# Performance work log

Hardware: AMD Instinct MI355X
Metric: run time of the kernel (lower is better)

## Reference

```python
import jax, jax.numpy as jnp
import numpy as np

KS = 3
N = KS * KS  # 9 kernel taps
EPS = 1e-5
LEAK = 0.1


def _conv2d(x, w, b=None, stride=1, pad=1):
    out = jax.lax.conv_general_dilated(
        x, w, (stride, stride), [(pad, pad), (pad, pad)],
        dimension_numbers=('NCHW', 'OIHW', 'NCHW'))
    if b is not None:
        out = out + b[None, :, None, None]
    return out


def setup_inputs() -> dict:
    key = jax.random.key(0)
    k1, k2, k3, k4 = jax.random.split(key, 4)
    b, c_in, c_out, H, W = 4, 128, 256, 128, 128
    x = jax.random.normal(k1, (b, c_in, H, W), dtype=jnp.float32)
    # offset-predicting conv (torch inits it to zero; small random keeps
    # sampling near-grid but nontrivial)
    p_w = jax.random.normal(k2, (2 * N, c_in, KS, KS), dtype=jnp.float32) * 0.01
    p_b = jnp.zeros((2 * N,), dtype=jnp.float32)
    # main conv weight (bias=False in DeformConv2d)
    w_conv = jax.random.normal(k3, (c_out, c_in, KS, KS), dtype=jnp.float32) * 0.05
    gamma = jnp.ones((c_out,), dtype=jnp.float32)
    beta = jnp.zeros((c_out,), dtype=jnp.float32)
    return {"x": x, "p_w": p_w, "p_b": p_b, "w_conv": w_conv,
            "gamma": gamma, "beta": beta}


def reference(x, p_w, p_b, w_conv, gamma, beta):
    b, c, H, W = x.shape
    # offsets: (b, 2N, H, W); first N channels = x-offsets, last N = y-offsets
    off = jnp.transpose(_conv2d(x, p_w, p_b), (0, 2, 3, 1))  # (b,h,w,2N)
    off_x, off_y = off[..., :N], off[..., N:]

    x_pad = jnp.pad(x, ((0, 0), (0, 0), (1, 1), (1, 1)))  # zero_padding(1)
    Hp, Wp = H + 2, W + 2

    # p = p_0 + p_n + offset (in padded coordinates)
    dx = jnp.repeat(jnp.arange(-1, 2), KS).astype(x.dtype)  # (9,)
    dy = jnp.tile(jnp.arange(-1, 2), KS).astype(x.dtype)
    p0x = jnp.arange(1, H + 1, dtype=x.dtype)[None, :, None, None]
    p0y = jnp.arange(1, W + 1, dtype=x.dtype)[None, None, :, None]
    px = p0x + dx + off_x  # (b,h,w,N)
    py = p0y + dy + off_y

    fx, fy = jnp.floor(px), jnp.floor(py)
    qlt_x = jnp.clip(fx, 0, Hp - 1)
    qlt_y = jnp.clip(fy, 0, Wp - 1)
    qrb_x = jnp.clip(fx + 1, 0, Hp - 1)
    qrb_y = jnp.clip(fy + 1, 0, Wp - 1)

    pcx = jnp.clip(px, 0, Hp - 1)
    pcy = jnp.clip(py, 0, Wp - 1)

    # bilinear weights (matches original g_lt/g_rb/g_lb/g_rt)
    g_lt = (1 + (qlt_x - pcx)) * (1 + (qlt_y - pcy))
    g_rb = (1 - (qrb_x - pcx)) * (1 - (qrb_y - pcy))
    g_lb = (1 + (qlt_x - pcx)) * (1 - (qrb_y - pcy))
    g_rt = (1 - (qrb_x - pcx)) * (1 + (qlt_y - pcy))

    x_flat = x_pad.reshape(b, c, Hp * Wp)
    ilt_x, ilt_y = qlt_x.astype(jnp.int32), qlt_y.astype(jnp.int32)
    irb_x, irb_y = qrb_x.astype(jnp.int32), qrb_y.astype(jnp.int32)

    def samp(ix, iy, g):
        idx = (ix * Wp + iy).reshape(b, -1)  # (b, h*w*N)
        v = jnp.take_along_axis(x_flat, idx[:, None, :], axis=2)
        return g[:, None] * v.reshape(b, c, H, W, N)

    x_off = (samp(ilt_x, ilt_y, g_lt) + samp(irb_x, irb_y, g_rb)
             + samp(ilt_x, irb_y, g_lb) + samp(irb_x, ilt_y, g_rt))

    # equivalent to reshaping to (b,c,3h,3w) and conv(k=3,s=3), bias=False
    out = jnp.einsum('bchwn,ocn->bohw', x_off,
                     w_conv.reshape(w_conv.shape[0], c, N))

    # BatchNorm2d (training-mode batch stats, biased var) + LeakyReLU(0.1)
    mean = out.mean(axis=(0, 2, 3), keepdims=True)
    var = ((out - mean) ** 2).mean(axis=(0, 2, 3), keepdims=True)
    out = (out - mean) * jax.lax.rsqrt(var + EPS)
    out = out * gamma[None, :, None, None] + beta[None, :, None, None]
    return jnp.where(out >= 0, out, LEAK * out)
```

## Files before the change

kernel.cpp:

```cpp
#include <hip/hip_runtime.h>
#include <cstdint>

typedef __attribute__((ext_vector_type(8))) short bf16x8;
typedef __attribute__((ext_vector_type(4))) float f32x4;

#define B_   4
#define C_   128
#define H_   128
#define W_   128
#define HP_  130
#define WP_  130
#define O_   256
#define HW_  (H_*W_)

#define XPAD_BYTES   (B_*HP_*WP_*C_*2)
#define OFF_BYTE     XPAD_BYTES
#define OFF_BYTES    (B_*HW_*18*4)
#define WREPB_BYTE   (OFF_BYTE + OFF_BYTES)
#define WREPB_BYTES  (9*C_*O_*2)
#define STATS_BYTE   (WREPB_BYTE + WREPB_BYTES)
#define WOFF_BYTE    (STATS_BYTE + 4096)
#define WOFF_BYTES   (9*4*4*32*8*2)

typedef __attribute__((address_space(1))) const void gconst_void;
typedef __attribute__((address_space(3))) void lds_void;
#define GLD_LDS16(gp, lp) __builtin_amdgcn_global_load_lds((gconst_void*)(gp), (lds_void*)(lp), 16, 0, 0)

__device__ __forceinline__ unsigned pack_bf2(float a, float b) {
    unsigned ua = __builtin_bit_cast(unsigned, a) + 0x8000u;
    unsigned ub = __builtin_bit_cast(unsigned, b) + 0x8000u;
    return __builtin_amdgcn_perm(ub, ua, 0x07060302u);
}

__global__ void k_transpose(const float* __restrict__ x, unsigned short* __restrict__ xpad) {
    __shared__ float tile[32][33];
    int w0 = blockIdx.x * 32, c0 = blockIdx.y * 32;
    int bh = blockIdx.z;
    int b = bh >> 7, h = bh & 127;
    int tx = threadIdx.x, ty = threadIdx.y;
#pragma unroll
    for (int i = 0; i < 4; i++) {
        int c = c0 + ty + i * 8;
        tile[ty + i * 8][tx] = x[((b * C_ + c) * H_ + h) * W_ + w0 + tx];
    }
    __syncthreads();
    int tid = ty * 32 + tx;
    int cp = tid & 15;
    int wl = tid >> 4;
#pragma unroll
    for (int i = 0; i < 2; i++) {
        int wll = wl + i * 16;
        int w = w0 + wll;
        unsigned v = pack_bf2(tile[2 * cp][wll], tile[2 * cp + 1][wll]);
        *(unsigned*)(&xpad[((size_t)((b * HP_ + h + 1) * WP_ + (w + 1))) * C_ + c0 + 2 * cp]) = v;
    }
}

__global__ void k_repack2(const float* __restrict__ p_w, short* __restrict__ wofff) {
    int i = blockIdx.x * 256 + threadIdx.x;
    if (i < 9 * 4096) {
        int e = i & 7, m = (i >> 3) & 31, q = (i >> 8) & 3, kc = (i >> 10) & 3, tap = i >> 12;
        float f = (m < 18) ? p_w[((size_t)m * C_ + kc * 32 + q * 8 + e) * 9 + tap] : 0.f;
        unsigned u = __builtin_bit_cast(unsigned, f);
        u += 0x7fffu + ((u >> 16) & 1u);
        wofff[i] = (short)(u >> 16);
    }
}

__global__ __launch_bounds__(256) void k_offconv(const unsigned short* __restrict__ xpad,
                                                 const short* __restrict__ wofff,
                                                 const float* __restrict__ p_b,
                                                 float* __restrict__ offT) {
    int t = threadIdx.x;
    int ph = blockIdx.x;
    int h  = blockIdx.y;
    int b  = blockIdx.z;
    const unsigned short* xb = xpad + (size_t)b * HP_ * WP_ * C_;
    int lane = t & 63, wv = t >> 6;
    int q = lane >> 4, l15 = lane & 15;
    int pos0 = ph * 64 + wv * 16;
    int poscol = pos0 + l15;

    f32x4 accA = {0.f, 0.f, 0.f, 0.f}, accB = {0.f, 0.f, 0.f, 0.f};
    const bf16x8* Wf = (const bf16x8*)wofff;

    for (int tap = 0; tap < 9; tap++) {
        int row = h + tap / 3;
        int col = poscol + tap % 3;
        const unsigned short* src = xb + ((size_t)(row * WP_ + col)) * C_ + q * 8;
#pragma unroll
        for (int kc = 0; kc < 4; kc++) {
            bf16x8 a0 = Wf[(size_t)(((tap * 4 + kc) * 4 + q) * 32) + l15];
            bf16x8 a1 = Wf[(size_t)(((tap * 4 + kc) * 4 + q) * 32) + 16 + l15];
            bf16x8 bv = *(const bf16x8*)(src + kc * 32);
            accA = __builtin_amdgcn_mfma_f32_16x16x32_bf16(a0, bv, accA, 0, 0, 0);
            accB = __builtin_amdgcn_mfma_f32_16x16x32_bf16(a1, bv, accB, 0, 0, 0);
        }
    }
    size_t hw = (size_t)h * W_ + pos0 + l15;
#pragma unroll
    for (int r = 0; r < 4; r++) {
        int j = q * 4 + r;
        offT[((size_t)(b * 18 + j)) * HW_ + hw] = accA[r] + p_b[j];
    }
    if (q == 0) {
#pragma unroll
        for (int r = 0; r < 2; r++) {
            int j = 16 + r;
            offT[((size_t)(b * 18 + j)) * HW_ + hw] = accB[r] + p_b[j];
        }
    }
}

__global__ void k_repack(const float* __restrict__ w_conv, unsigned short* __restrict__ wrepb) {
    int i = blockIdx.x * 256 + threadIdx.x;
    if (i < 9 * C_ * O_) {
        int ki8 = i & 7;
        int o   = (i >> 3) & 255;
        int kq  = (i >> 11) & 3;
        int kc  = (i >> 13) & 3;
        int n   = i >> 15;
        int c = kc * 32 + kq * 8 + ki8;
        float f = w_conv[(o * C_ + c) * 9 + n];
        unsigned u = __builtin_bit_cast(unsigned, f);
        u += 0x7fffu + ((u >> 16) & 1u);
        wrepb[i] = (unsigned short)(u >> 16);
    }
}

__global__ __launch_bounds__(512, 4) void k_main(const unsigned short* __restrict__ xpad,
                                                 const float* __restrict__ offT,
                                                 const unsigned short* __restrict__ wrepb,
                                                 float* __restrict__ out,
                                                 float* __restrict__ stats) {
    __shared__ short Wl[2][8192];
    __shared__ short Vl[2][4128];
    __shared__ int   pbase[2][4][128];
    __shared__ float pg[2][4][128];
    __shared__ float red0[256], red1[256];

    int t = threadIdx.x;
    int i_blk = blockIdx.x;
    int b = i_blk & 3;
    int h = i_blk >> 2;
    const unsigned short* xb = xpad + (size_t)b * HP_ * WP_ * C_;

    int lane = t & 63, wv = t >> 6;
    int q = lane >> 4, l15 = lane & 15;
    int m0 = (wv & 3) * 64;
    int ph = wv >> 2;
    int n0 = ph * 64;
    int c4g = t & 3, posb = t >> 2;

    auto OFFSETS = [&](int n, int pb) {
        if (t < 128) {
            int w = t;
            float offx = offT[((size_t)(b * 18 + n)) * HW_ + h * W_ + w];
            float offy = offT[((size_t)(b * 18 + 9 + n)) * HW_ + h * W_ + w];
            int dxn = n / 3 - 1, dyn = n % 3 - 1;
            float px = (float)(h + 1 + dxn) + offx;
            float py = (float)(w + 1 + dyn) + offy;
            float pcx = fminf(fmaxf(px, 0.f), 129.f);
            float pcy = fminf(fmaxf(py, 0.f), 129.f);
            float fx = floorf(px), fy = floorf(py);
            float q0x = fminf(fmaxf(fx, 0.f), 129.f);
            float q0y = fminf(fmaxf(fy, 0.f), 129.f);
            float q1x = fminf(fmaxf(fx + 1.f, 0.f), 129.f);
            float q1y = fminf(fmaxf(fy + 1.f, 0.f), 129.f);
            float wx0 = 1.f + (q0x - pcx), wx1 = 1.f - (q1x - pcx);
            float wy0 = 1.f + (q0y - pcy), wy1 = 1.f - (q1y - pcy);
            int i0x = (int)q0x, i0y = (int)q0y, i1x = (int)q1x, i1y = (int)q1y;
            pbase[pb][0][w] = (i0x * WP_ + i0y) * C_;
            pbase[pb][1][w] = (i1x * WP_ + i1y) * C_;
            pbase[pb][2][w] = (i0x * WP_ + i1y) * C_;
            pbase[pb][3][w] = (i1x * WP_ + i0y) * C_;
            pg[pb][0][w] = wx0 * wy0;
            pg[pb][1][w] = wx1 * wy1;
            pg[pb][2][w] = wx0 * wy1;
            pg[pb][3][w] = wx1 * wy0;
        }
    };

    f32x4 acc[4][4];
#pragma unroll
    for (int i = 0; i < 4; i++)
#pragma unroll
        for (int j = 0; j < 4; j++) acc[i][j] = (f32x4){0.f, 0.f, 0.f, 0.f};

    OFFSETS(0, 0);
    __syncthreads();

    {
        const unsigned short* ws = wrepb;
        GLD_LDS16(ws + (size_t)t * 8, &Wl[0][wv * 512]);
        GLD_LDS16(ws + (size_t)(t + 512) * 8, &Wl[0][wv * 512 + 4096]);
        int cof = c4g * 8;
        uint4 A  = *(const uint4*)(xb + pbase[0][0][posb] + cof);
        uint4 Bv = *(const uint4*)(xb + pbase[0][1][posb] + cof);
        uint4 Cv = *(const uint4*)(xb + pbase[0][2][posb] + cof);
        uint4 Dv = *(const uint4*)(xb + pbase[0][3][posb] + cof);
        float g0 = pg[0][0][posb], g1 = pg[0][1][posb], g2 = pg[0][2][posb], g3 = pg[0][3][posb];
        unsigned outw[4];
#pragma unroll
        for (int k = 0; k < 4; k++) {
            unsigned ua = (&A.x)[k], ub = (&Bv.x)[k], uc = (&Cv.x)[k], ud = (&Dv.x)[k];
            float alo = __builtin_bit_cast(float, ua << 16), ahi = __builtin_bit_cast(float, ua & 0xffff0000u);
            float blo = __builtin_bit_cast(float, ub << 16), bhi = __builtin_bit_cast(float, ub & 0xffff0000u);
            float clo = __builtin_bit_cast(float, uc << 16), chi = __builtin_bit_cast(float, uc & 0xffff0000u);
            float dlo = __builtin_bit_cast(float, ud << 16), dhi = __builtin_bit_cast(float, ud & 0xffff0000u);
            float vlo = g0 * alo + g1 * blo + g2 * clo + g3 * dlo;
            float vhi = g0 * ahi + g1 * bhi + g2 * chi + g3 * dhi;
            outw[k] = pack_bf2(vlo, vhi);
        }
        *(uint4*)&Vl[0][(unsigned)(c4g * 129 + posb) * 8] = make_uint4(outw[0], outw[1], outw[2], outw[3]);
    }
    __syncthreads();

#pragma unroll 1
    for (int s = 0; s < 36; s++) {
        int cur = s & 1, nxt = cur ^ 1;
        uint4 A, Bv, Cv, Dv;
        float g0 = 0.f, g1 = 0.f, g2 = 0.f, g3 = 0.f;
        bool st = (s < 35);
        if (st) {
            int s1 = s + 1;
            const unsigned short* ws = wrepb + (size_t)s1 * 8192;
            GLD_LDS16(ws + (size_t)t * 8, &Wl[nxt][wv * 512]);
            GLD_LDS16(ws + (size_t)(t + 512) * 8, &Wl[nxt][wv * 512 + 4096]);
            int n1 = s1 >> 2, kc1 = s1 & 3, pb1 = n1 & 1;
            int cof = kc1 * 32 + c4g * 8;
            A  = *(const uint4*)(xb + pbase[pb1][0][posb] + cof);
            Bv = *(const uint4*)(xb + pbase[pb1][1][posb] + cof);
            Cv = *(const uint4*)(xb + pbase[pb1][2][posb] + cof);
            Dv = *(const uint4*)(xb + pbase[pb1][3][posb] + cof);
            g0 = pg[pb1][0][posb]; g1 = pg[pb1][1][posb];
            g2 = pg[pb1][2][posb]; g3 = pg[pb1][3][posb];
        }
        {
            const bf16x8* Af = (const bf16x8*)Wl[cur];
            const bf16x8* Bf = (const bf16x8*)Vl[cur];
            bf16x8 av[4];
#pragma unroll
            for (int i = 0; i < 4; i++) av[i] = Af[q * 256 + m0 + i * 16 + l15];
            __builtin_amdgcn_s_setprio(1);
#pragma unroll
            for (int j = 0; j < 4; j++) {
                bf16x8 bv = Bf[q * 129 + n0 + j * 16 + l15];
#pragma unroll
                for (int i = 0; i < 4; i++)
                    acc[i][j] = __builtin_amdgcn_mfma_f32_16x16x32_bf16(av[i], bv, acc[i][j], 0, 0, 0);
            }
            __builtin_amdgcn_s_setprio(0);
        }
        if ((s & 3) == 2) {
            int n = s >> 2;
            if (n < 8) OFFSETS(n + 1, (n + 1) & 1);
        }
        if (st) {
            unsigned outw[4];
#pragma unroll
            for (int k = 0; k < 4; k++) {
                unsigned ua = (&A.x)[k], ub = (&Bv.x)[k], uc = (&Cv.x)[k], ud = (&Dv.x)[k];
                float alo = __builtin_bit_cast(float, ua << 16), ahi = __builtin_bit_cast(float, ua & 0xffff0000u);
                float blo = __builtin_bit_cast(float, ub << 16), bhi = __builtin_bit_cast(float, ub & 0xffff0000u);
                float clo = __builtin_bit_cast(float, uc << 16), chi = __builtin_bit_cast(float, uc & 0xffff0000u);
                float dlo = __builtin_bit_cast(float, ud << 16), dhi = __builtin_bit_cast(float, ud & 0xffff0000u);
                float vlo = g0 * alo + g1 * blo + g2 * clo + g3 * dlo;
                float vhi = g0 * ahi + g1 * bhi + g2 * chi + g3 * dhi;
                outw[k] = pack_bf2(vlo, vhi);
            }
            *(uint4*)&Vl[nxt][(unsigned)(c4g * 129 + posb) * 8] = make_uint4(outw[0], outw[1], outw[2], outw[3]);
        }
        __syncthreads();
    }

    if (t < 256) { red0[t] = 0.f; red1[t] = 0.f; }
    __syncthreads();
#pragma unroll
    for (int i = 0; i < 4; i++) {
#pragma unroll
        for (int r = 0; r < 4; r++) {
            int o_loc = m0 + i * 16 + q * 4 + r;
            float s = 0.f, s2 = 0.f;
#pragma unroll
            for (int j = 0; j < 4; j++) { float v = acc[i][j][r]; s += v; s2 += v * v; }
            s  += __shfl_xor(s, 1);  s  += __shfl_xor(s, 2);  s  += __shfl_xor(s, 4);  s  += __shfl_xor(s, 8);
            s2 += __shfl_xor(s2, 1); s2 += __shfl_xor(s2, 2); s2 += __shfl_xor(s2, 4); s2 += __shfl_xor(s2, 8);
            if (l15 == 0) { atomicAdd(&red0[o_loc], s); atomicAdd(&red1[o_loc], s2); }
        }
    }
    __syncthreads();
    if (t < 256) {
        atomicAdd(&stats[t], red0[t]);
        atomicAdd(&stats[256 + t], red1[t]);
    }

    float* outb = out + ((size_t)b * O_) * HW_ + (size_t)h * W_;
#pragma unroll
    for (int i = 0; i < 4; i++)
#pragma unroll
        for (int j = 0; j < 4; j++) {
            int col = ph * 64 + j * 16 + l15;
#pragma unroll
            for (int r = 0; r < 4; r++) {
                int o = m0 + i * 16 + q * 4 + r;
                outb[(size_t)o * HW_ + col] = acc[i][j][r];
            }
        }
}

__global__ void k_bnstats(float* __restrict__ stats,
                          const float* __restrict__ gamma,
                          const float* __restrict__ beta) {
    int t = threadIdx.x;
    float s = stats[t], s2 = stats[256 + t];
    float mean = s * (1.f / 65536.f);
    float var = s2 * (1.f / 65536.f) - mean * mean;
    float sc = gamma[t] * rsqrtf(var + 1e-5f);
    float sh = beta[t] - mean * sc;
    stats[512 + t] = sc;
    stats[768 + t] = sh;
}

__global__ __launch_bounds__(256) void k_apply(float* __restrict__ out,
                                               const float* __restrict__ stats) {
    int idx = blockIdx.x * 256 + threadIdx.x;
    int e = idx * 4;
    int o = (e >> 14) & 255;
    float sc = stats[512 + o], sh = stats[768 + o];
    float4 v = *(float4*)(out + e);
    v.x = v.x * sc + sh; v.x = (v.x >= 0.f) ? v.x : 0.1f * v.x;
    v.y = v.y * sc + sh; v.y = (v.y >= 0.f) ? v.y : 0.1f * v.y;
    v.z = v.z * sc + sh; v.z = (v.z >= 0.f) ? v.z : 0.1f * v.z;
    v.w = v.w * sc + sh; v.w = (v.w >= 0.f) ? v.w : 0.1f * v.w;
    *(float4*)(out + e) = v;
}

extern "C" void kernel_launch(void* const* d_in, const int* in_sizes, int n_in,
                              void* d_out, int out_size, void* d_ws, size_t ws_size,
                              hipStream_t stream) {
    const float* x      = (const float*)d_in[0];
    const float* p_w    = (const float*)d_in[1];
    const float* p_b    = (const float*)d_in[2];
    const float* w_conv = (const float*)d_in[3];
    const float* gamma  = (const float*)d_in[4];
    const float* beta   = (const float*)d_in[5];
    float* out = (float*)d_out;

    char* wsb = (char*)d_ws;
    unsigned short* xpad  = (unsigned short*)wsb;
    float*          offT  = (float*)(wsb + OFF_BYTE);
    unsigned short* wrepb = (unsigned short*)(wsb + WREPB_BYTE);
    float*          stats = (float*)(wsb + STATS_BYTE);
    short*          wofff = (short*)(wsb + WOFF_BYTE);

    hipMemsetAsync(xpad, 0, (size_t)XPAD_BYTES, stream);
    hipMemsetAsync(stats, 0, 4096, stream);

    k_transpose<<<dim3(W_ / 32, C_ / 32, B_ * H_), dim3(32, 8), 0, stream>>>(x, xpad);
    k_repack2<<<dim3(144), 256, 0, stream>>>(p_w, wofff);
    k_offconv<<<dim3(2, H_, B_), 256, 0, stream>>>(xpad, wofff, p_b, offT);
    k_repack<<<dim3((9 * C_ * O_ + 255) / 256), 256, 0, stream>>>(w_conv, wrepb);
    k_main<<<dim3(512), 512, 0, stream>>>(xpad, offT, wrepb, out, stats);
    k_bnstats<<<1, 256, 0, stream>>>(stats, gamma, beta);
    k_apply<<<dim3(16384), 256, 0, stream>>>(out, stats);
}
```

Before: 230.0 us.

## Deepen gather prefetch to two stages with explicit waitcnt barriers

Bilinear-sampling gathers are now issued two K-steps ahead into two alternating register sets, so each set is blended one step after its loads were issued. __syncthreads is replaced with hand-written s_waitcnt vmcnt(4)/lgkmcnt(0) plus s_barrier, with sched_barriers fencing the regions, so the outstanding gather loads do not have to drain at every step. The OFFSETS computation moves one step earlier to stay ahead of the deeper prefetch. This trades more live registers and a fragile manual wait count for more latency hiding of the global gathers.

```diff
diff --git a/kernel.cpp b/kernel.cpp
--- a/kernel.cpp
+++ b/kernel.cpp
@@ -181,29 +181,26 @@
         }
     };
 
-    f32x4 acc[4][4];
-#pragma unroll
-    for (int i = 0; i < 4; i++)
-#pragma unroll
-        for (int j = 0; j < 4; j++) acc[i][j] = (f32x4){0.f, 0.f, 0.f, 0.f};
-
-    OFFSETS(0, 0);
-    __syncthreads();
-
-    {
-        const unsigned short* ws = wrepb;
-        GLD_LDS16(ws + (size_t)t * 8, &Wl[0][wv * 512]);
-        GLD_LDS16(ws + (size_t)(t + 512) * 8, &Wl[0][wv * 512 + 4096]);
-        int cof = c4g * 8;
-        uint4 A  = *(const uint4*)(xb + pbase[0][0][posb] + cof);
-        uint4 Bv = *(const uint4*)(xb + pbase[0][1][posb] + cof);
-        uint4 Cv = *(const uint4*)(xb + pbase[0][2][posb] + cof);
-        uint4 Dv = *(const uint4*)(xb + pbase[0][3][posb] + cof);
-        float g0 = pg[0][0][posb], g1 = pg[0][1][posb], g2 = pg[0][2][posb], g3 = pg[0][3][posb];
+    struct GSet { uint4 A, B, C, D; };
+    GSet ga, gb;
+
+    auto GISSUE = [&](GSet& g, int s2) {
+        int pb = (s2 >> 2) & 1;
+        int cof = (s2 & 3) * 32 + c4g * 8;
+        g.A = *(const uint4*)(xb + pbase[pb][0][posb] + cof);
+        g.B = *(const uint4*)(xb + pbase[pb][1][posb] + cof);
+        g.C = *(const uint4*)(xb + pbase[pb][2][posb] + cof);
+        g.D = *(const uint4*)(xb + pbase[pb][3][posb] + cof);
+    };
+
+    auto BLEND = [&](GSet& g, int sb, int buf) {
+        int pb = (sb >> 2) & 1;
+        float g0 = pg[pb][0][posb], g1 = pg[pb][1][posb];
+        float g2 = pg[pb][2][posb], g3 = pg[pb][3][posb];
         unsigned outw[4];
 #pragma unroll
         for (int k = 0; k < 4; k++) {
-            unsigned ua = (&A.x)[k], ub = (&Bv.x)[k], uc = (&Cv.x)[k], ud = (&Dv.x)[k];
+            unsigned ua = (&g.A.x)[k], ub = (&g.B.x)[k], uc = (&g.C.x)[k], ud = (&g.D.x)[k];
             float alo = __builtin_bit_cast(float, ua << 16), ahi = __builtin_bit_cast(float, ua & 0xffff0000u);
             float blo = __builtin_bit_cast(float, ub << 16), bhi = __builtin_bit_cast(float, ub & 0xffff0000u);
             float clo = __builtin_bit_cast(float, uc << 16), chi = __builtin_bit_cast(float, uc & 0xffff0000u);
@@ -212,30 +209,37 @@
             float vhi = g0 * ahi + g1 * bhi + g2 * chi + g3 * dhi;
             outw[k] = pack_bf2(vlo, vhi);
         }
-        *(uint4*)&Vl[0][(unsigned)(c4g * 129 + posb) * 8] = make_uint4(outw[0], outw[1], outw[2], outw[3]);
-    }
-    __syncthreads();
-
-#pragma unroll 1
-    for (int s = 0; s < 36; s++) {
+        *(uint4*)&Vl[buf][(unsigned)(c4g * 129 + posb) * 8] = make_uint4(outw[0], outw[1], outw[2], outw[3]);
+    };
+
+    f32x4 acc[4][4];
+#pragma unroll
+    for (int i = 0; i < 4; i++)
+#pragma unroll
+        for (int j = 0; j < 4; j++) acc[i][j] = (f32x4){0.f, 0.f, 0.f, 0.f};
+
+    OFFSETS(0, 0);
+    __syncthreads();
+
+    {
+        const unsigned short* ws = wrepb;
+        GLD_LDS16(ws + (size_t)t * 8, &Wl[0][wv * 512]);
+        GLD_LDS16(ws + (size_t)(t + 512) * 8, &Wl[0][wv * 512 + 4096]);
+        GISSUE(ga, 0);
+        BLEND(ga, 0, 0);
+        GISSUE(ga, 1);
+    }
+    __syncthreads();
+
+    auto STEP = [&](GSet& pend, GSet& fill, int s, int vm) {
         int cur = s & 1, nxt = cur ^ 1;
-        uint4 A, Bv, Cv, Dv;
-        float g0 = 0.f, g1 = 0.f, g2 = 0.f, g3 = 0.f;
-        bool st = (s < 35);
-        if (st) {
-            int s1 = s + 1;
-            const unsigned short* ws = wrepb + (size_t)s1 * 8192;
+        if (s <= 34) {
+            const unsigned short* ws = wrepb + (size_t)(s + 1) * 8192;
             GLD_LDS16(ws + (size_t)t * 8, &Wl[nxt][wv * 512]);
             GLD_LDS16(ws + (size_t)(t + 512) * 8, &Wl[nxt][wv * 512 + 4096]);
-            int n1 = s1 >> 2, kc1 = s1 & 3, pb1 = n1 & 1;
-            int cof = kc1 * 32 + c4g * 8;
-            A  = *(const uint4*)(xb + pbase[pb1][0][posb] + cof);
-            Bv = *(const uint4*)(xb + pbase[pb1][1][posb] + cof);
-            Cv = *(const uint4*)(xb + pbase[pb1][2][posb] + cof);
-            Dv = *(const uint4*)(xb + pbase[pb1][3][posb] + cof);
-            g0 = pg[pb1][0][posb]; g1 = pg[pb1][1][posb];
-            g2 = pg[pb1][2][posb]; g3 = pg[pb1][3][posb];
-        }
+        }
+        __builtin_amdgcn_sched_barrier(0);
+        if (s <= 33) GISSUE(fill, s + 2);
         {
             const bf16x8* Af = (const bf16x8*)Wl[cur];
             const bf16x8* Bf = (const bf16x8*)Vl[cur];
@@ -252,27 +256,24 @@
             }
             __builtin_amdgcn_s_setprio(0);
         }
-        if ((s & 3) == 2) {
-            int n = s >> 2;
-            if (n < 8) OFFSETS(n + 1, (n + 1) & 1);
-        }
-        if (st) {
-            unsigned outw[4];
-#pragma unroll
-            for (int k = 0; k < 4; k++) {
-                unsigned ua = (&A.x)[k], ub = (&Bv.x)[k], uc = (&Cv.x)[k], ud = (&Dv.x)[k];
-                float alo = __builtin_bit_cast(float, ua << 16), ahi = __builtin_bit_cast(float, ua & 0xffff0000u);
-                float blo = __builtin_bit_cast(float, ub << 16), bhi = __builtin_bit_cast(float, ub & 0xffff0000u);
-                float clo = __builtin_bit_cast(float, uc << 16), chi = __builtin_bit_cast(float, uc & 0xffff0000u);
-                float dlo = __builtin_bit_cast(float, ud << 16), dhi = __builtin_bit_cast(float, ud & 0xffff0000u);
-                float vlo = g0 * alo + g1 * blo + g2 * clo + g3 * dlo;
-                float vhi = g0 * ahi + g1 * bhi + g2 * chi + g3 * dhi;
-                outw[k] = pack_bf2(vlo, vhi);
-            }
-            *(uint4*)&Vl[nxt][(unsigned)(c4g * 129 + posb) * 8] = make_uint4(outw[0], outw[1], outw[2], outw[3]);
-        }
-        __syncthreads();
-    }
+        if ((s & 3) == 1) {
+            int n1 = (s >> 2) + 1;
+            if (n1 <= 8) OFFSETS(n1, n1 & 1);
+        }
+        if (s <= 34) BLEND(pend, s + 1, nxt);
+        __builtin_amdgcn_sched_barrier(0);
+        if (vm == 4) asm volatile("s_waitcnt vmcnt(4) lgkmcnt(0)" ::: "memory");
+        else         asm volatile("s_waitcnt vmcnt(0) lgkmcnt(0)" ::: "memory");
+        __builtin_amdgcn_s_barrier();
+        __builtin_amdgcn_sched_barrier(0);
+    };
+
+    for (int s = 0; s < 34; s += 2) {
+        STEP(ga, gb, s, 4);
+        STEP(gb, ga, s + 1, 4);
+    }
+    STEP(ga, gb, 34, 0);
+    STEP(gb, ga, 35, 0);
 
     if (t < 256) { red0[t] = 0.f; red1[t] = 0.f; }
     __syncthreads();
```

Measured after the change: 251.4 us. 9.3% more time.

## Fuse BatchNorm stats and apply into main kernel via grid barrier; merge repacks

Applied to the files above, without the earlier changes.

Replaces the separate BN-stats and BN-apply/LeakyReLU kernels with a software grid-wide barrier at the end of k_main. Blocks spin on an atomic counter until all 512 have added their partial sums, then each block normalises its register-resident accumulators and writes the final output once. This removes a full extra read and write of the 64 MB output plus two launches. The two weight repack kernels are also merged into one launch. The barrier relies on all 512 blocks being co-resident, otherwise it deadlocks. The counter lives in the stats buffer that is zeroed each call.

```diff
diff --git a/kernel.cpp b/kernel.cpp
--- a/kernel.cpp
+++ b/kernel.cpp
@@ -56,7 +56,8 @@
     }
 }
 
-__global__ void k_repack2(const float* __restrict__ p_w, short* __restrict__ wofff) {
+__global__ void k_repackA(const float* __restrict__ p_w, short* __restrict__ wofff,
+                          const float* __restrict__ w_conv, unsigned short* __restrict__ wrepb) {
     int i = blockIdx.x * 256 + threadIdx.x;
     if (i < 9 * 4096) {
         int e = i & 7, m = (i >> 3) & 31, q = (i >> 8) & 3, kc = (i >> 10) & 3, tap = i >> 12;
@@ -64,6 +65,19 @@
         unsigned u = __builtin_bit_cast(unsigned, f);
         u += 0x7fffu + ((u >> 16) & 1u);
         wofff[i] = (short)(u >> 16);
+    }
+    int j = i - 9 * 4096;
+    if (j >= 0 && j < 9 * C_ * O_) {
+        int ki8 = j & 7;
+        int o   = (j >> 3) & 255;
+        int kq  = (j >> 11) & 3;
+        int kc  = (j >> 13) & 3;
+        int n   = j >> 15;
+        int c = kc * 32 + kq * 8 + ki8;
+        float f = w_conv[(o * C_ + c) * 9 + n];
+        unsigned u = __builtin_bit_cast(unsigned, f);
+        u += 0x7fffu + ((u >> 16) & 1u);
+        wrepb[j] = (unsigned short)(u >> 16);
     }
 }
 
@@ -112,27 +126,13 @@
     }
 }
 
-__global__ void k_repack(const float* __restrict__ w_conv, unsigned short* __restrict__ wrepb) {
-    int i = blockIdx.x * 256 + threadIdx.x;
-    if (i < 9 * C_ * O_) {
-        int ki8 = i & 7;
-        int o   = (i >> 3) & 255;
-        int kq  = (i >> 11) & 3;
-        int kc  = (i >> 13) & 3;
-        int n   = i >> 15;
-        int c = kc * 32 + kq * 8 + ki8;
-        float f = w_conv[(o * C_ + c) * 9 + n];
-        unsigned u = __builtin_bit_cast(unsigned, f);
-        u += 0x7fffu + ((u >> 16) & 1u);
-        wrepb[i] = (unsigned short)(u >> 16);
-    }
-}
-
 __global__ __launch_bounds__(512, 4) void k_main(const unsigned short* __restrict__ xpad,
                                                  const float* __restrict__ offT,
                                                  const unsigned short* __restrict__ wrepb,
                                                  float* __restrict__ out,
-                                                 float* __restrict__ stats) {
+                                                 float* __restrict__ stats,
+                                                 const float* __restrict__ gamma,
+                                                 const float* __restrict__ beta) {
     __shared__ short Wl[2][8192];
     __shared__ short Vl[2][4128];
     __shared__ int   pbase[2][4][128];
@@ -294,46 +294,43 @@
         atomicAdd(&stats[t], red0[t]);
         atomicAdd(&stats[256 + t], red1[t]);
     }
+    __syncthreads();
+
+    unsigned* cnt = (unsigned*)(stats + 1020);
+    if (t == 0) {
+        __threadfence();
+        __hip_atomic_fetch_add(cnt, 1u, __ATOMIC_RELEASE, __HIP_MEMORY_SCOPE_AGENT);
+        while (__hip_atomic_load(cnt, __ATOMIC_ACQUIRE, __HIP_MEMORY_SCOPE_AGENT) < 512u)
+            __builtin_amdgcn_s_sleep(8);
+    }
+    __syncthreads();
+
+    if (t < 256) {
+        float s0  = __hip_atomic_load(&stats[t],       __ATOMIC_RELAXED, __HIP_MEMORY_SCOPE_AGENT);
+        float s2v = __hip_atomic_load(&stats[256 + t], __ATOMIC_RELAXED, __HIP_MEMORY_SCOPE_AGENT);
+        float mean = s0 * (1.f / 65536.f);
+        float var = s2v * (1.f / 65536.f) - mean * mean;
+        float sc = gamma[t] * rsqrtf(var + 1e-5f);
+        red0[t] = sc;
+        red1[t] = beta[t] - mean * sc;
+    }
+    __syncthreads();
 
     float* outb = out + ((size_t)b * O_) * HW_ + (size_t)h * W_;
 #pragma unroll
     for (int i = 0; i < 4; i++)
 #pragma unroll
-        for (int j = 0; j < 4; j++) {
-            int col = ph * 64 + j * 16 + l15;
-#pragma unroll
-            for (int r = 0; r < 4; r++) {
-                int o = m0 + i * 16 + q * 4 + r;
-                outb[(size_t)o * HW_ + col] = acc[i][j][r];
+        for (int r = 0; r < 4; r++) {
+            int o = m0 + i * 16 + q * 4 + r;
+            float sc = red0[o], sh = red1[o];
+#pragma unroll
+            for (int j = 0; j < 4; j++) {
+                int col = ph * 64 + j * 16 + l15;
+                float v = acc[i][j][r] * sc + sh;
+                v = (v >= 0.f) ? v : 0.1f * v;
+                outb[(size_t)o * HW_ + col] = v;
             }
         }
-}
-
-__global__ void k_bnstats(float* __restrict__ stats,
-                          const float* __restrict__ gamma,
-                          const float* __restrict__ beta) {
-    int t = threadIdx.x;
-    float s = stats[t], s2 = stats[256 + t];
-    float mean = s * (1.f / 65536.f);
-    float var = s2 * (1.f / 65536.f) - mean * mean;
-    float sc = gamma[t] * rsqrtf(var + 1e-5f);
-    float sh = beta[t] - mean * sc;
-    stats[512 + t] = sc;
-    stats[768 + t] = sh;
-}
-
-__global__ __launch_bounds__(256) void k_apply(float* __restrict__ out,
-                                               const float* __restrict__ stats) {
-    int idx = blockIdx.x * 256 + threadIdx.x;
-    int e = idx * 4;
-    int o = (e >> 14) & 255;
-    float sc = stats[512 + o], sh = stats[768 + o];
-    float4 v = *(float4*)(out + e);
-    v.x = v.x * sc + sh; v.x = (v.x >= 0.f) ? v.x : 0.1f * v.x;
-    v.y = v.y * sc + sh; v.y = (v.y >= 0.f) ? v.y : 0.1f * v.y;
-    v.z = v.z * sc + sh; v.z = (v.z >= 0.f) ? v.z : 0.1f * v.z;
-    v.w = v.w * sc + sh; v.w = (v.w >= 0.f) ? v.w : 0.1f * v.w;
-    *(float4*)(out + e) = v;
 }
 
 extern "C" void kernel_launch(void* const* d_in, const int* in_sizes, int n_in,
@@ -358,10 +355,7 @@
     hipMemsetAsync(stats, 0, 4096, stream);
 
     k_transpose<<<dim3(W_ / 32, C_ / 32, B_ * H_), dim3(32, 8), 0, stream>>>(x, xpad);
-    k_repack2<<<dim3(144), 256, 0, stream>>>(p_w, wofff);
+    k_repackA<<<dim3((9 * 4096 + 9 * C_ * O_ + 255) / 256), 256, 0, stream>>>(p_w, wofff, w_conv, wrepb);
     k_offconv<<<dim3(2, H_, B_), 256, 0, stream>>>(xpad, wofff, p_b, offT);
-    k_repack<<<dim3((9 * C_ * O_ + 255) / 256), 256, 0, stream>>>(w_conv, wrepb);
-    k_main<<<dim3(512), 512, 0, stream>>>(xpad, offT, wrepb, out, stats);
-    k_bnstats<<<1, 256, 0, stream>>>(stats, gamma, beta);
-    k_apply<<<dim3(16384), 256, 0, stream>>>(out, stats);
-}
+    k_main<<<dim3(512), 512, 0, stream>>>(xpad, offT, wrepb, out, stats, gamma, beta);
+}
```

After: 251.2 us. 1.09x slower.
